# Performance work log

Hardware: AMD Instinct MI355X
Metric: run time of the kernel (lower is better)

Reference implementation:

```python
import jax, jax.numpy as jnp
import numpy as np

NF, NC, LENGTH, BATCH = 64, 16, 2048, 256
WEIGHT_BI, WEIGHT_L2 = 0.01, 0.01
BETA = 2.5     # temporal soft-min/max sharpness (TemporalOperator beta=2.5)
KAPPA = 10.0   # logical soft-min/max sharpness (avm approximation)
EPSN = 1e-12


def setup_inputs() -> dict:
    key = jax.random.key(0)
    ks = jax.random.split(key, 11)
    x = jax.random.normal(ks[0], (BATCH, LENGTH, 2), dtype=jnp.float32)
    t1 = jax.random.uniform(ks[1], (NF,), minval=0.0, maxval=float(LENGTH // 2), dtype=jnp.float32)
    t2 = jax.random.uniform(ks[2], (NF,), minval=float(LENGTH // 2), maxval=float(LENGTH), dtype=jnp.float32)
    a = jax.random.uniform(ks[3], (NF,), dtype=jnp.float32)
    b = jax.random.uniform(ks[4], (NF,), dtype=jnp.float32)
    p1 = jax.random.uniform(ks[5], (NC, NF), dtype=jnp.float32)
    p2 = jax.random.uniform(ks[6], (1, NC), dtype=jnp.float32)
    tvar_temporal = jax.random.uniform(ks[7], (NF,), dtype=jnp.float32)
    tvar_logical1 = jax.random.uniform(ks[8], (NC,), dtype=jnp.float32)
    tvar_logical2 = jax.random.uniform(ks[9], (1,), dtype=jnp.float32)
    eps = jnp.full((1,), 0.1, dtype=jnp.float32)
    return dict(x=x, t1=t1, t2=t2, a=a, b=b, p1=p1, p2=p2,
                tvar_temporal=tvar_temporal, tvar_logical1=tvar_logical1,
                tvar_logical2=tvar_logical2, eps=eps)


def _ste(v, v_new):
    # torch clamps parameter .data under no_grad -> value changes, grad is identity
    return v + jax.lax.stop_gradient(v_new - v)


def _wsel(r, logw, sharp):
    # weighted soft-max (sharp>0) / soft-min (sharp<0) along last axis
    s = jax.nn.softmax(sharp * r + logw, axis=-1)
    return jnp.sum(s * r, axis=-1)


def reference(x, t1, t2, a, b, p1, p2, tvar_temporal, tvar_logical1, tvar_logical2, eps):
    # --- in-place parameter maintenance (clamp under no_grad in torch) ---
    p1 = _ste(p1, jnp.clip(p1, 0.0, 1.0))
    p2 = _ste(p2, jnp.clip(p2, 0.0, 1.0))
    tvt = _ste(tvar_temporal, jnp.clip(tvar_temporal, 0.0, 1.0))
    tvl1 = _ste(tvar_logical1, jnp.clip(tvar_logical1, 0.0, 1.0))
    tvl2 = _ste(tvar_logical2, jnp.clip(tvar_logical2, 0.0, 1.0))
    t1c = jnp.clip(t1, 0.0, LENGTH - 1.0)
    t2c = jnp.clip(t2, 0.0, LENGTH - 1.0)
    t1c = jnp.where(t1c >= t2c - 1.0, t2c - 1.0, t1c)
    t1u = _ste(t1, t1c)
    t2u = _ste(t2, t2c)

    # --- predicates (vectorized over all nf features; dim = i % 2) ---
    dims = jnp.arange(NF) % 2
    rp = a[None, None, :] * x[:, :, dims] - b[None, None, :]     # [B, T, NF]
    rp = jnp.transpose(rp, (0, 2, 1))                             # [B, NF, T]

    # --- temporal operators: smooth window [t1, t2] + soft min/max over time ---
    tg = jnp.arange(LENGTH, dtype=x.dtype)
    w = jax.nn.sigmoid(BETA * (tg[None, :] - t1u[:, None])) * \
        jax.nn.sigmoid(BETA * (t2u[:, None] - tg[None, :]))       # [NF, T]
    logw = jnp.log(w + EPSN)[None]                                # [1, NF, T]
    rmax = _wsel(rp, logw, BETA)                                  # eventually  [B, NF]
    rmin = _wsel(rp, logw, -BETA)                                 # always      [B, NF]
    r1 = tvt[None, :] * rmax + (1.0 - tvt[None, :]) * rmin        # [B, NF]

    # --- logical layer 1: weighted soft OR/AND over features, per clause ---
    logp1 = jnp.log(p1 + EPSN)[None]                              # [1, NC, NF]
    r1e = r1[:, None, :]                                          # [B, NC, NF]
    r_or = _wsel(r1e, logp1, KAPPA)
    r_and = _wsel(r1e, logp1, -KAPPA)
    r2 = tvl1[None, :] * r_or + (1.0 - tvl1[None, :]) * r_and     # [B, NC]

    # --- logical layer 2: combine clauses ---
    logp2 = jnp.log(p2[0] + EPSN)[None]                           # [1, NC]
    r_or2 = _wsel(r2, logp2, KAPPA)
    r_and2 = _wsel(r2, logp2, -KAPPA)
    r = tvl2[0] * r_or2 + (1.0 - tvl2[0]) * r_and2                # [B]

    # --- regularizers ---
    bi = WEIGHT_BI * (jnp.sum(tvt * (1.0 - tvt)) + jnp.sum(tvl1 * (1.0 - tvl1)) +
                      jnp.sum(tvl2 * (1.0 - tvl2)) + jnp.sum(p1 * (1.0 - p1)) +
                      jnp.sum(p2 * (1.0 - p2)))
    l2 = WEIGHT_L2 * (jnp.sum(p1 * p1) + jnp.sum(p2 * p2))
    reg = bi + l2
    return r, reg
```

## Files before the change

### kernel.cpp

```cpp
#include <hip/hip_runtime.h>
#include <math.h>

#define NF 64
#define NC 16
#define LEN 2048
#define BATCH 256
#define BETA 2.5f
#define KAPPA 10.0f
#define EPSN 1e-12f
#define LOG2E 1.4426950408889634f

#define SPLIT 2
#define HALF (LEN / SPLIT)
#define TPB 1024
#define NQ (TPB / NF)
#define CHUNK (HALF / NQ)
#define CHUNK_MONO (LEN / NQ)

__device__ __forceinline__ float clip01(float v) { return fminf(fmaxf(v, 0.0f), 1.0f); }

__device__ __forceinline__ float fexp2(float x) {
#if __has_builtin(__builtin_amdgcn_exp2f)
    return __builtin_amdgcn_exp2f(x);
#else
    return exp2f(x);
#endif
}

__global__ void lw_kernel(const float* __restrict__ t1, const float* __restrict__ t2,
                          float* __restrict__ lwT) {
    int idx = blockIdx.x * blockDim.x + threadIdx.x;
    if (idx >= NF * LEN) return;
    int f = idx & (NF - 1);
    int t = idx >> 6;
    float t1c = fminf(fmaxf(t1[f], 0.0f), (float)(LEN - 1));
    float t2c = fminf(fmaxf(t2[f], 0.0f), (float)(LEN - 1));
    t1c = fminf(t1c, t2c - 1.0f);
    float su = 1.0f / (1.0f + __expf(-BETA * ((float)t - t1c)));
    float sv = 1.0f / (1.0f + __expf(-BETA * (t2c - (float)t)));
    lwT[idx] = __log2f(su * sv + EPSN);
}

__global__ __launch_bounds__(TPB) void main_split(
    const float* __restrict__ x, const float* __restrict__ av,
    const float* __restrict__ bv, const float* __restrict__ lwT,
    float4* __restrict__ part) {
    __shared__ float xs[HALF * 2];
    __shared__ float4 redQ[NQ][NF];

    const int b = blockIdx.x >> 1;
    const int h = blockIdx.x & 1;
    const int tid = threadIdx.x;
    const int f = tid & (NF - 1);
    const int q = tid >> 6;

    ((float2*)xs)[tid] = ((const float2*)(x + (size_t)b * (LEN * 2) + h * (HALF * 2)))[tid];

    const float a = av[f];
    const float bb = bv[f];
    const int ch = f & 1;
    const float B2 = BETA * LOG2E;

    __syncthreads();

    const int lt0 = q * CHUNK;
    const int gt0 = h * HALF + lt0;

    float sp = 0.f, wp = 0.f, sm = 0.f, wm = 0.f;
#pragma unroll 8
    for (int k = 0; k < CHUNK; ++k) {
        float lw2 = lwT[(gt0 + k) * NF + f];
        float xv = xs[2 * (lt0 + k) + ch];
        float rp = fmaf(a, xv, -bb);
        float ep = fexp2(fmaf(B2, rp, lw2));
        float em = fexp2(fmaf(-B2, rp, lw2));
        sp += ep;
        wp = fmaf(ep, rp, wp);
        sm += em;
        wm = fmaf(em, rp, wm);
    }
    redQ[q][f] = make_float4(sp, wp, sm, wm);
    __syncthreads();

    if (q == 0) {
        float Sp = 0.f, Wp = 0.f, Sm = 0.f, Wm = 0.f;
#pragma unroll
        for (int j = 0; j < NQ; ++j) {
            float4 v = redQ[j][f];
            Sp += v.x; Wp += v.y; Sm += v.z; Wm += v.w;
        }
        part[(size_t)h * BATCH * NF + (size_t)b * NF + f] = make_float4(Sp, Wp, Sm, Wm);
    }
}

__global__ __launch_bounds__(64) void finish_kernel(
    const float4* __restrict__ part, const float* __restrict__ p1,
    const float* __restrict__ p2, const float* __restrict__ tvt_,
    const float* __restrict__ tvl1_, const float* __restrict__ tvl2_,
    float* __restrict__ out) {
    __shared__ float r1s[NF];
    __shared__ float lp[NC][NF];
    __shared__ float r2s[NC];

    const int b = blockIdx.x;
    const int f = threadIdx.x;
    const float KL = KAPPA * LOG2E;

    float4 A = part[(size_t)b * NF + f];
    float4 Bq = part[(size_t)BATCH * NF + (size_t)b * NF + f];
    float Sp = A.x + Bq.x, Wp = A.y + Bq.y, Sm = A.z + Bq.z, Wm = A.w + Bq.w;
    float tvt = clip01(tvt_[f]);
    r1s[f] = tvt * (Wp / Sp) + (1.0f - tvt) * (Wm / Sm);

#pragma unroll
    for (int c = 0; c < NC; ++c)
        lp[c][f] = __log2f(clip01(p1[c * NF + f]) + EPSN);
    __syncthreads();

    if (f < NC) {
        const int c = f;
        float mo = -INFINITY, ma = -INFINITY;
#pragma unroll
        for (int ff = 0; ff < NF; ++ff) {
            float z = KL * r1s[ff];
            float l = lp[c][ff];
            mo = fmaxf(mo, z + l);
            ma = fmaxf(ma, l - z);
        }
        float so = 0.f, wo = 0.f, sa = 0.f, wa = 0.f;
#pragma unroll
        for (int ff = 0; ff < NF; ++ff) {
            float r1v = r1s[ff];
            float z = KL * r1v;
            float l = lp[c][ff];
            float eo = fexp2(z + l - mo);
            float ea = fexp2(l - z - ma);
            so += eo; wo = fmaf(eo, r1v, wo);
            sa += ea; wa = fmaf(ea, r1v, wa);
        }
        float tvl1 = clip01(tvl1_[c]);
        r2s[c] = tvl1 * (wo / so) + (1.0f - tvl1) * (wa / sa);
    }
    __syncthreads();

    if (f == 0) {
        float mo = -INFINITY, ma = -INFINITY;
#pragma unroll
        for (int c = 0; c < NC; ++c) {
            float l = __log2f(clip01(p2[c]) + EPSN);
            float z = KL * r2s[c];
            mo = fmaxf(mo, z + l);
            ma = fmaxf(ma, l - z);
        }
        float so = 0.f, wo = 0.f, sa = 0.f, wa = 0.f;
#pragma unroll
        for (int c = 0; c < NC; ++c) {
            float l = __log2f(clip01(p2[c]) + EPSN);
            float r2v = r2s[c];
            float z = KL * r2v;
            float eo = fexp2(z + l - mo);
            float ea = fexp2(l - z - ma);
            so += eo; wo = fmaf(eo, r2v, wo);
            sa += ea; wa = fmaf(ea, r2v, wa);
        }
        float tvl2 = clip01(tvl2_[0]);
        out[b] = tvl2 * (wo / so) + (1.0f - tvl2) * (wa / sa);
    }
}

template <bool USE_WS>
__global__ __launch_bounds__(TPB) void main_mono(
    const float* __restrict__ x, const float* __restrict__ av,
    const float* __restrict__ bv, const float* __restrict__ lwT,
    const float* __restrict__ t1g, const float* __restrict__ t2g,
    const float* __restrict__ p1, const float* __restrict__ p2,
    const float* __restrict__ tvt_, const float* __restrict__ tvl1_,
    const float* __restrict__ tvl2_, float* __restrict__ out) {
    __shared__ float xs[LEN * 2];
    __shared__ float4 redQ[NQ][NF];
    __shared__ float lp[NC][NF];
    __shared__ float r1s[NF];
    __shared__ float r2s[NC];

    const int b = blockIdx.x;
    const int tid = threadIdx.x;
    const int f = tid & (NF - 1);
    const int q = tid >> 6;
    const float B2 = BETA * LOG2E;
    const float KL = KAPPA * LOG2E;

    ((float4*)xs)[tid] = ((const float4*)(x + (size_t)b * (LEN * 2)))[tid];

    const float a = av[f];
    const float bb = bv[f];
    const int ch = f & 1;

    float t1c = 0.f, t2c = 0.f;
    if (!USE_WS) {
        t1c = fminf(fmaxf(t1g[f], 0.0f), (float)(LEN - 1));
        t2c = fminf(fmaxf(t2g[f], 0.0f), (float)(LEN - 1));
        t1c = fminf(t1c, t2c - 1.0f);
    }
    __syncthreads();

    const int t0 = q * CHUNK_MONO;
    float sp = 0.f, wp = 0.f, sm = 0.f, wm = 0.f;
#pragma unroll 8
    for (int k = 0; k < CHUNK_MONO; ++k) {
        int t = t0 + k;
        float lw2;
        if (USE_WS) {
            lw2 = lwT[t * NF + f];
        } else {
            float su = 1.0f / (1.0f + __expf(-BETA * ((float)t - t1c)));
            float sv = 1.0f / (1.0f + __expf(-BETA * (t2c - (float)t)));
            lw2 = __log2f(su * sv + EPSN);
        }
        float xv = xs[2 * t + ch];
        float rp = fmaf(a, xv, -bb);
        float ep = fexp2(fmaf(B2, rp, lw2));
        float em = fexp2(fmaf(-B2, rp, lw2));
        sp += ep; wp = fmaf(ep, rp, wp);
        sm += em; wm = fmaf(em, rp, wm);
    }
    redQ[q][f] = make_float4(sp, wp, sm, wm);
    {
        float pv = clip01(p1[tid]);
        ((float*)lp)[tid] = __log2f(pv + EPSN);
    }
    __syncthreads();

    if (q == 0) {
        float Sp = 0.f, Wp = 0.f, Sm = 0.f, Wm = 0.f;
#pragma unroll
        for (int j = 0; j < NQ; ++j) {
            float4 v = redQ[j][f];
            Sp += v.x; Wp += v.y; Sm += v.z; Wm += v.w;
        }
        float tvt = clip01(tvt_[f]);
        r1s[f] = tvt * (Wp / Sp) + (1.0f - tvt) * (Wm / Sm);
    }
    __syncthreads();

    if (tid < NC) {
        const int c = tid;
        float mo = -INFINITY, ma = -INFINITY;
#pragma unroll
        for (int ff = 0; ff < NF; ++ff) {
            float z = KL * r1s[ff];
            float l = lp[c][ff];
            mo = fmaxf(mo, z + l);
            ma = fmaxf(ma, l - z);
        }
        float so = 0.f, wo = 0.f, sa = 0.f, wa = 0.f;
#pragma unroll
        for (int ff = 0; ff < NF; ++ff) {
            float r1v = r1s[ff];
            float z = KL * r1v;
            float l = lp[c][ff];
            float eo = fexp2(z + l - mo);
            float ea = fexp2(l - z - ma);
            so += eo; wo = fmaf(eo, r1v, wo);
            sa += ea; wa = fmaf(ea, r1v, wa);
        }
        float tvl1 = clip01(tvl1_[c]);
        r2s[c] = tvl1 * (wo / so) + (1.0f - tvl1) * (wa / sa);
    }
    __syncthreads();

    if (tid == 0) {
        float mo = -INFINITY, ma = -INFINITY;
#pragma unroll
        for (int c = 0; c < NC; ++c) {
            float l = __log2f(clip01(p2[c]) + EPSN);
            float z = KL * r2s[c];
            mo = fmaxf(mo, z + l);
            ma = fmaxf(ma, l - z);
        }
        float so = 0.f, wo = 0.f, sa = 0.f, wa = 0.f;
#pragma unroll
        for (int c = 0; c < NC; ++c) {
            float l = __log2f(clip01(p2[c]) + EPSN);
            float r2v = r2s[c];
            float z = KL * r2v;
            float eo = fexp2(z + l - mo);
            float ea = fexp2(l - z - ma);
            so += eo; wo = fmaf(eo, r2v, wo);
            sa += ea; wa = fmaf(ea, r2v, wa);
        }
        float tvl2 = clip01(tvl2_[0]);
        out[b] = tvl2 * (wo / so) + (1.0f - tvl2) * (wa / sa);
    }
}

__global__ void reg_kernel(const float* __restrict__ p1, const float* __restrict__ p2,
                           const float* __restrict__ tvt, const float* __restrict__ tvl1,
                           const float* __restrict__ tvl2, float* __restrict__ out) {
    __shared__ float red[256];
    int tid = threadIdx.x;
    float acc = 0.0f;
    for (int i = tid; i < NC * NF; i += 256) {
        float p = clip01(p1[i]);
        acc += 0.01f * (p * (1.0f - p)) + 0.01f * (p * p);
    }
    if (tid < NC) {
        float p = clip01(p2[tid]);
        acc += 0.01f * (p * (1.0f - p)) + 0.01f * (p * p);
    }
    if (tid < NF) {
        float c = clip01(tvt[tid]);
        acc += 0.01f * (c * (1.0f - c));
    }
    if (tid < NC) {
        float c = clip01(tvl1[tid]);
        acc += 0.01f * (c * (1.0f - c));
    }
    if (tid == 0) {
        float c = clip01(tvl2[0]);
        acc += 0.01f * (c * (1.0f - c));
    }
    red[tid] = acc;
    __syncthreads();
    for (int s = 128; s > 0; s >>= 1) {
        if (tid < s) red[tid] += red[tid + s];
        __syncthreads();
    }
    if (tid == 0) out[BATCH] = red[0];
}

extern "C" void kernel_launch(void* const* d_in, const int* in_sizes, int n_in,
                              void* d_out, int out_size, void* d_ws, size_t ws_size,
                              hipStream_t stream) {
    const float* x    = (const float*)d_in[0];
    const float* t1   = (const float*)d_in[1];
    const float* t2   = (const float*)d_in[2];
    const float* a    = (const float*)d_in[3];
    const float* bv   = (const float*)d_in[4];
    const float* p1   = (const float*)d_in[5];
    const float* p2   = (const float*)d_in[6];
    const float* tvt  = (const float*)d_in[7];
    const float* tvl1 = (const float*)d_in[8];
    const float* tvl2 = (const float*)d_in[9];
    float* out = (float*)d_out;

    const size_t lw_bytes = (size_t)(NF * LEN) * sizeof(float);
    const size_t part_bytes = (size_t)SPLIT * BATCH * NF * sizeof(float4);

    if (d_ws && ws_size >= lw_bytes + part_bytes) {
        float* lwT = (float*)d_ws;
        float4* part = (float4*)((char*)d_ws + lw_bytes);
        lw_kernel<<<(NF * LEN + 255) / 256, 256, 0, stream>>>(t1, t2, lwT);
        main_split<<<BATCH * SPLIT, TPB, 0, stream>>>(x, a, bv, lwT, part);
        finish_kernel<<<BATCH, 64, 0, stream>>>(part, p1, p2, tvt, tvl1, tvl2, out);
    } else if (d_ws && ws_size >= lw_bytes) {
        float* lwT = (float*)d_ws;
        lw_kernel<<<(NF * LEN + 255) / 256, 256, 0, stream>>>(t1, t2, lwT);
        main_mono<true><<<BATCH, TPB, 0, stream>>>(x, a, bv, lwT, t1, t2, p1, p2,
                                                   tvt, tvl1, tvl2, out);
    } else {
        main_mono<false><<<BATCH, TPB, 0, stream>>>(x, a, bv, nullptr, t1, t2, p1, p2,
                                                    tvt, tvl1, tvl2, out);
    }
    reg_kernel<<<1, 256, 0, stream>>>(p1, p2, tvt, tvl1, tvl2, out);
}
```

Measured before the change: 28.53 us.

## Fuse reg into lw kernel, move split reduction to finish, drop max pass

Folds the regularizer computation into an extra block of the lw table kernel, which removes one kernel launch. The main split kernel no longer does its in-block shared-memory reduction and barrier: each quarter-wave group writes its own partial, and the finish kernel sums all 32 partials per batch. The finish stages also drop the max-subtraction pass in the logical soft-min/max. That is safe only while KAPPA*r stays within fp32 exp range, so it risks overflow for large activations. The mono fallback that read the workspace is removed.

```diff
diff --git a/kernel.cpp b/kernel.cpp
--- a/kernel.cpp
+++ b/kernel.cpp
@@ -14,6 +14,7 @@
 #define HALF (LEN / SPLIT)
 #define TPB 1024
 #define NQ (TPB / NF)
+#define NS (SPLIT * NQ)
 #define CHUNK (HALF / NQ)
 #define CHUNK_MONO (LEN / NQ)
 
@@ -27,10 +28,49 @@
 #endif
 }
 
-__global__ void lw_kernel(const float* __restrict__ t1, const float* __restrict__ t2,
-                          float* __restrict__ lwT) {
-    int idx = blockIdx.x * blockDim.x + threadIdx.x;
-    if (idx >= NF * LEN) return;
+__global__ __launch_bounds__(256) void lw_reg_kernel(
+    const float* __restrict__ t1, const float* __restrict__ t2,
+    const float* __restrict__ p1, const float* __restrict__ p2,
+    const float* __restrict__ tvt, const float* __restrict__ tvl1,
+    const float* __restrict__ tvl2, float* __restrict__ lwT,
+    float* __restrict__ out) {
+    const int bid = blockIdx.x;
+    const int tid = threadIdx.x;
+
+    if (bid == (NF * LEN) / 256) {
+        __shared__ float red[256];
+        float acc = 0.0f;
+        for (int i = tid; i < NC * NF; i += 256) {
+            float p = clip01(p1[i]);
+            acc += 0.01f * (p * (1.0f - p)) + 0.01f * (p * p);
+        }
+        if (tid < NC) {
+            float p = clip01(p2[tid]);
+            acc += 0.01f * (p * (1.0f - p)) + 0.01f * (p * p);
+        }
+        if (tid < NF) {
+            float c = clip01(tvt[tid]);
+            acc += 0.01f * (c * (1.0f - c));
+        }
+        if (tid < NC) {
+            float c = clip01(tvl1[tid]);
+            acc += 0.01f * (c * (1.0f - c));
+        }
+        if (tid == 0) {
+            float c = clip01(tvl2[0]);
+            acc += 0.01f * (c * (1.0f - c));
+        }
+        red[tid] = acc;
+        __syncthreads();
+        for (int s = 128; s > 0; s >>= 1) {
+            if (tid < s) red[tid] += red[tid + s];
+            __syncthreads();
+        }
+        if (tid == 0) out[BATCH] = red[0];
+        return;
+    }
+
+    int idx = bid * 256 + tid;
     int f = idx & (NF - 1);
     int t = idx >> 6;
     float t1c = fminf(fmaxf(t1[f], 0.0f), (float)(LEN - 1));
@@ -46,7 +86,6 @@
     const float* __restrict__ bv, const float* __restrict__ lwT,
     float4* __restrict__ part) {
     __shared__ float xs[HALF * 2];
-    __shared__ float4 redQ[NQ][NF];
 
     const int b = blockIdx.x >> 1;
     const int h = blockIdx.x & 1;
@@ -64,12 +103,12 @@
     __syncthreads();
 
     const int lt0 = q * CHUNK;
-    const int gt0 = h * HALF + lt0;
+    const float* lwp = lwT + (size_t)(h * HALF + lt0) * NF + f;
 
     float sp = 0.f, wp = 0.f, sm = 0.f, wm = 0.f;
 #pragma unroll 8
     for (int k = 0; k < CHUNK; ++k) {
-        float lw2 = lwT[(gt0 + k) * NF + f];
+        float lw2 = lwp[k * NF];
         float xv = xs[2 * (lt0 + k) + ch];
         float rp = fmaf(a, xv, -bb);
         float ep = fexp2(fmaf(B2, rp, lw2));
@@ -79,18 +118,9 @@
         sm += em;
         wm = fmaf(em, rp, wm);
     }
-    redQ[q][f] = make_float4(sp, wp, sm, wm);
-    __syncthreads();
-
-    if (q == 0) {
-        float Sp = 0.f, Wp = 0.f, Sm = 0.f, Wm = 0.f;
-#pragma unroll
-        for (int j = 0; j < NQ; ++j) {
-            float4 v = redQ[j][f];
-            Sp += v.x; Wp += v.y; Sm += v.z; Wm += v.w;
-        }
-        part[(size_t)h * BATCH * NF + (size_t)b * NF + f] = make_float4(Sp, Wp, Sm, Wm);
-    }
+
+    const int s = h * NQ + q;
+    part[((size_t)b * NS + s) * NF + f] = make_float4(sp, wp, sm, wm);
 }
 
 __global__ __launch_bounds__(64) void finish_kernel(
@@ -106,9 +136,12 @@
     const int f = threadIdx.x;
     const float KL = KAPPA * LOG2E;
 
-    float4 A = part[(size_t)b * NF + f];
-    float4 Bq = part[(size_t)BATCH * NF + (size_t)b * NF + f];
-    float Sp = A.x + Bq.x, Wp = A.y + Bq.y, Sm = A.z + Bq.z, Wm = A.w + Bq.w;
+    float Sp = 0.f, Wp = 0.f, Sm = 0.f, Wm = 0.f;
+#pragma unroll
+    for (int s = 0; s < NS; ++s) {
+        float4 v = part[((size_t)b * NS + s) * NF + f];
+        Sp += v.x; Wp += v.y; Sm += v.z; Wm += v.w;
+    }
     float tvt = clip01(tvt_[f]);
     r1s[f] = tvt * (Wp / Sp) + (1.0f - tvt) * (Wm / Sm);
 
@@ -119,22 +152,14 @@
 
     if (f < NC) {
         const int c = f;
-        float mo = -INFINITY, ma = -INFINITY;
-#pragma unroll
-        for (int ff = 0; ff < NF; ++ff) {
-            float z = KL * r1s[ff];
-            float l = lp[c][ff];
-            mo = fmaxf(mo, z + l);
-            ma = fmaxf(ma, l - z);
-        }
         float so = 0.f, wo = 0.f, sa = 0.f, wa = 0.f;
 #pragma unroll
         for (int ff = 0; ff < NF; ++ff) {
             float r1v = r1s[ff];
             float z = KL * r1v;
             float l = lp[c][ff];
-            float eo = fexp2(z + l - mo);
-            float ea = fexp2(l - z - ma);
+            float eo = fexp2(z + l);
+            float ea = fexp2(l - z);
             so += eo; wo = fmaf(eo, r1v, wo);
             sa += ea; wa = fmaf(ea, r1v, wa);
         }
@@ -144,22 +169,14 @@
     __syncthreads();
 
     if (f == 0) {
-        float mo = -INFINITY, ma = -INFINITY;
-#pragma unroll
-        for (int c = 0; c < NC; ++c) {
-            float l = __log2f(clip01(p2[c]) + EPSN);
-            float z = KL * r2s[c];
-            mo = fmaxf(mo, z + l);
-            ma = fmaxf(ma, l - z);
-        }
         float so = 0.f, wo = 0.f, sa = 0.f, wa = 0.f;
 #pragma unroll
         for (int c = 0; c < NC; ++c) {
             float l = __log2f(clip01(p2[c]) + EPSN);
             float r2v = r2s[c];
             float z = KL * r2v;
-            float eo = fexp2(z + l - mo);
-            float ea = fexp2(l - z - ma);
+            float eo = fexp2(z + l);
+            float ea = fexp2(l - z);
             so += eo; wo = fmaf(eo, r2v, wo);
             sa += ea; wa = fmaf(ea, r2v, wa);
         }
@@ -168,10 +185,9 @@
     }
 }
 
-template <bool USE_WS>
 __global__ __launch_bounds__(TPB) void main_mono(
     const float* __restrict__ x, const float* __restrict__ av,
-    const float* __restrict__ bv, const float* __restrict__ lwT,
+    const float* __restrict__ bv,
     const float* __restrict__ t1g, const float* __restrict__ t2g,
     const float* __restrict__ p1, const float* __restrict__ p2,
     const float* __restrict__ tvt_, const float* __restrict__ tvl1_,
@@ -195,12 +211,9 @@
     const float bb = bv[f];
     const int ch = f & 1;
 
-    float t1c = 0.f, t2c = 0.f;
-    if (!USE_WS) {
-        t1c = fminf(fmaxf(t1g[f], 0.0f), (float)(LEN - 1));
-        t2c = fminf(fmaxf(t2g[f], 0.0f), (float)(LEN - 1));
-        t1c = fminf(t1c, t2c - 1.0f);
-    }
+    float t1c = fminf(fmaxf(t1g[f], 0.0f), (float)(LEN - 1));
+    float t2c = fminf(fmaxf(t2g[f], 0.0f), (float)(LEN - 1));
+    t1c = fminf(t1c, t2c - 1.0f);
     __syncthreads();
 
     const int t0 = q * CHUNK_MONO;
@@ -208,14 +221,9 @@
 #pragma unroll 8
     for (int k = 0; k < CHUNK_MONO; ++k) {
         int t = t0 + k;
-        float lw2;
-        if (USE_WS) {
-            lw2 = lwT[t * NF + f];
-        } else {
-            float su = 1.0f / (1.0f + __expf(-BETA * ((float)t - t1c)));
-            float sv = 1.0f / (1.0f + __expf(-BETA * (t2c - (float)t)));
-            lw2 = __log2f(su * sv + EPSN);
-        }
+        float su = 1.0f / (1.0f + __expf(-BETA * ((float)t - t1c)));
+        float sv = 1.0f / (1.0f + __expf(-BETA * (t2c - (float)t)));
+        float lw2 = __log2f(su * sv + EPSN);
         float xv = xs[2 * t + ch];
         float rp = fmaf(a, xv, -bb);
         float ep = fexp2(fmaf(B2, rp, lw2));
@@ -244,22 +252,14 @@
 
     if (tid < NC) {
         const int c = tid;
-        float mo = -INFINITY, ma = -INFINITY;
-#pragma unroll
-        for (int ff = 0; ff < NF; ++ff) {
-            float z = KL * r1s[ff];
-            float l = lp[c][ff];
-            mo = fmaxf(mo, z + l);
-            ma = fmaxf(ma, l - z);
-        }
         float so = 0.f, wo = 0.f, sa = 0.f, wa = 0.f;
 #pragma unroll
         for (int ff = 0; ff < NF; ++ff) {
             float r1v = r1s[ff];
             float z = KL * r1v;
             float l = lp[c][ff];
-            float eo = fexp2(z + l - mo);
-            float ea = fexp2(l - z - ma);
+            float eo = fexp2(z + l);
+            float ea = fexp2(l - z);
             so += eo; wo = fmaf(eo, r1v, wo);
             sa += ea; wa = fmaf(ea, r1v, wa);
         }
@@ -269,22 +269,14 @@
     __syncthreads();
 
     if (tid == 0) {
-        float mo = -INFINITY, ma = -INFINITY;
-#pragma unroll
-        for (int c = 0; c < NC; ++c) {
-            float l = __log2f(clip01(p2[c]) + EPSN);
-            float z = KL * r2s[c];
-            mo = fmaxf(mo, z + l);
-            ma = fmaxf(ma, l - z);
-        }
         float so = 0.f, wo = 0.f, sa = 0.f, wa = 0.f;
 #pragma unroll
         for (int c = 0; c < NC; ++c) {
             float l = __log2f(clip01(p2[c]) + EPSN);
             float r2v = r2s[c];
             float z = KL * r2v;
-            float eo = fexp2(z + l - mo);
-            float ea = fexp2(l - z - ma);
+            float eo = fexp2(z + l);
+            float ea = fexp2(l - z);
             so += eo; wo = fmaf(eo, r2v, wo);
             sa += ea; wa = fmaf(ea, r2v, wa);
         }
@@ -344,22 +336,18 @@
     float* out = (float*)d_out;
 
     const size_t lw_bytes = (size_t)(NF * LEN) * sizeof(float);
-    const size_t part_bytes = (size_t)SPLIT * BATCH * NF * sizeof(float4);
+    const size_t part_bytes = (size_t)BATCH * NS * NF * sizeof(float4);
 
     if (d_ws && ws_size >= lw_bytes + part_bytes) {
         float* lwT = (float*)d_ws;
         float4* part = (float4*)((char*)d_ws + lw_bytes);
-        lw_kernel<<<(NF * LEN + 255) / 256, 256, 0, stream>>>(t1, t2, lwT);
+        lw_reg_kernel<<<(NF * LEN) / 256 + 1, 256, 0, stream>>>(t1, t2, p1, p2, tvt, tvl1,
+                                                                tvl2, lwT, out);
         main_split<<<BATCH * SPLIT, TPB, 0, stream>>>(x, a, bv, lwT, part);
         finish_kernel<<<BATCH, 64, 0, stream>>>(part, p1, p2, tvt, tvl1, tvl2, out);
-    } else if (d_ws && ws_size >= lw_bytes) {
-        float* lwT = (float*)d_ws;
-        lw_kernel<<<(NF * LEN + 255) / 256, 256, 0, stream>>>(t1, t2, lwT);
-        main_mono<true><<<BATCH, TPB, 0, stream>>>(x, a, bv, lwT, t1, t2, p1, p2,
-                                                   tvt, tvl1, tvl2, out);
     } else {
-        main_mono<false><<<BATCH, TPB, 0, stream>>>(x, a, bv, nullptr, t1, t2, p1, p2,
-                                                    tvt, tvl1, tvl2, out);
-    }
-    reg_kernel<<<1, 256, 0, stream>>>(p1, p2, tvt, tvl1, tvl2, out);
-}
+        main_mono<<<BATCH, TPB, 0, stream>>>(x, a, bv, t1, t2, p1, p2,
+                                             tvt, tvl1, tvl2, out);
+        reg_kernel<<<1, 256, 0, stream>>>(p1, p2, tvt, tvl1, tvl2, out);
+    }
+}
```

Result: no change. 28.72 us (+0.7%).
